# Kernel optimization log

Hardware: AMD Instinct MI355X
Metric: run time of the kernel (lower is better)

Reference implementation:

```python
import jax, jax.numpy as jnp
import numpy as np

N_NODES = 100000
N_EDGES = 1600000
HIDDEN = 128


def setup_inputs() -> dict:
    key = jax.random.key(0)
    k1, k2, k3, k4 = jax.random.split(key, 4)
    x = jax.random.normal(k1, (N_NODES, HIDDEN), dtype=jnp.float32)
    edge_index = jax.random.randint(k2, (2, N_EDGES), 0, N_NODES, dtype=jnp.int64)
    edge_weight = jax.random.uniform(k3, (N_EDGES,), dtype=jnp.float32)
    W_att = jax.random.normal(k4, (1, HIDDEN), dtype=jnp.float32) * (1.0 / np.sqrt(HIDDEN))
    b_att = jnp.zeros((1,), dtype=jnp.float32)
    return {"x": x, "edge_index": edge_index, "edge_weight": edge_weight,
            "W_att": W_att, "b_att": b_att}


def reference(x, edge_index, edge_weight, W_att, b_att):
    row, col = edge_index[0], edge_index[1]
    # per-node attention score in (0,1): sigmoid(Linear(x))  -> [N]
    scores = jax.nn.sigmoid(x @ W_att.T + b_att)[:, 0]
    # per-edge energy: gather endpoints, multiply by edge weight  -> [E]
    energy = scores[row] * scores[col] * edge_weight
    # GLOBAL softmax over all edges (dim=0 in torch)  -> [E]
    attn = jax.nn.softmax(energy)
    # scatter-add weighted source features into row nodes  -> [N, H]
    out = jax.ops.segment_sum(x[col] * attn[:, None], row, num_segments=x.shape[0])
    return out
```

## Files before the change

### kernel.cpp

```cpp
#include <hip/hip_runtime.h>
#include <math.h>

#define N_NODES  100000
#define N_EDGES  1600000
#define HIDDEN   128
#define CAP      32
#define OVF_CAP  8192

__global__ void scores_kernel(const float* __restrict__ x,
                              const float* __restrict__ W,
                              const float* __restrict__ b,
                              float* __restrict__ scores) {
    int gwave = (blockIdx.x * blockDim.x + threadIdx.x) >> 6;
    int lane  = threadIdx.x & 63;
    if (gwave >= N_NODES) return;
    const float2 xv = *reinterpret_cast<const float2*>(x + (size_t)gwave * HIDDEN + lane * 2);
    const float2 wv = *reinterpret_cast<const float2*>(W + lane * 2);
    float d = xv.x * wv.x + xv.y * wv.y;
#pragma unroll
    for (int off = 32; off > 0; off >>= 1)
        d += __shfl_xor(d, off, 64);
    if (lane == 0) {
        float z = d + b[0];
        scores[gwave] = 1.0f / (1.0f + expf(-z));
    }
}

__global__ void energy_bucket_kernel(const int* __restrict__ ei,
                                     const float* __restrict__ ew,
                                     const float* __restrict__ scores,
                                     double* __restrict__ sum,
                                     int* __restrict__ cnt,
                                     float2* __restrict__ ebuf,
                                     int* __restrict__ ovf_cnt,
                                     float4* __restrict__ ovf) {
    int e4 = blockIdx.x * blockDim.x + threadIdx.x;
    double local = 0.0;
    if (e4 < N_EDGES / 4) {
        int4   r4 = reinterpret_cast<const int4*>(ei)[e4];
        int4   c4 = reinterpret_cast<const int4*>(ei + N_EDGES)[e4];
        float4 w4 = reinterpret_cast<const float4*>(ew)[e4];
        int   rs[4] = {r4.x, r4.y, r4.z, r4.w};
        int   cs[4] = {c4.x, c4.y, c4.z, c4.w};
        float wsv[4] = {w4.x, w4.y, w4.z, w4.w};
#pragma unroll
        for (int k = 0; k < 4; ++k) {
            int r = rs[k], c = cs[k];
            float pe = expf(scores[r] * scores[c] * wsv[k]);
            local += (double)pe;
            int pos = atomicAdd(&cnt[r], 1);
            if (pos < CAP) {
                ebuf[(size_t)r * CAP + pos] = make_float2(__int_as_float(c), pe);
            } else {
                int oi = atomicAdd(ovf_cnt, 1);
                if (oi < OVF_CAP)
                    ovf[oi] = make_float4(__int_as_float(r), __int_as_float(c), pe, 0.f);
            }
        }
    }
#pragma unroll
    for (int off = 32; off > 0; off >>= 1)
        local += __shfl_xor(local, off, 64);
    __shared__ double part[4];
    int lane = threadIdx.x & 63, w = threadIdx.x >> 6;
    if (lane == 0) part[w] = local;
    __syncthreads();
    if (threadIdx.x == 0)
        atomicAdd(sum, part[0] + part[1] + part[2] + part[3]);
}

__global__ void accumulate_kernel(const float* __restrict__ x,
                                  const int* __restrict__ cnt,
                                  const float2* __restrict__ ebuf,
                                  const double* __restrict__ sum,
                                  float* __restrict__ out) {
    int n    = (blockIdx.x * blockDim.x + threadIdx.x) >> 6;
    int lane = threadIdx.x & 63;
    if (n >= N_NODES) return;
    int deg = cnt[n];
    if (deg > CAP) deg = CAP;
    const float4* rec4 = reinterpret_cast<const float4*>(ebuf + (size_t)n * CAP);
    float a0 = 0.f, a1 = 0.f;
    int j = 0;
    for (; j + 4 <= deg; j += 4) {
        float4 q0 = rec4[(j >> 1)];
        float4 q1 = rec4[(j >> 1) + 1];
        const float2 x0 = *reinterpret_cast<const float2*>(x + (size_t)__float_as_int(q0.x) * HIDDEN + lane * 2);
        const float2 x1 = *reinterpret_cast<const float2*>(x + (size_t)__float_as_int(q0.z) * HIDDEN + lane * 2);
        const float2 x2 = *reinterpret_cast<const float2*>(x + (size_t)__float_as_int(q1.x) * HIDDEN + lane * 2);
        const float2 x3 = *reinterpret_cast<const float2*>(x + (size_t)__float_as_int(q1.z) * HIDDEN + lane * 2);
        a0 += x0.x * q0.y; a1 += x0.y * q0.y;
        a0 += x1.x * q0.w; a1 += x1.y * q0.w;
        a0 += x2.x * q1.y; a1 += x2.y * q1.y;
        a0 += x3.x * q1.w; a1 += x3.y * q1.w;
    }
    const float2* rec = ebuf + (size_t)n * CAP;
    for (; j < deg; ++j) {
        float2 r = rec[j];
        const float2 xv = *reinterpret_cast<const float2*>(x + (size_t)__float_as_int(r.x) * HIDDEN + lane * 2);
        a0 += xv.x * r.y; a1 += xv.y * r.y;
    }
    float inv = (float)(1.0 / sum[0]);
    *reinterpret_cast<float2*>(out + (size_t)n * HIDDEN + lane * 2) =
        make_float2(a0 * inv, a1 * inv);
}

__global__ void overflow_kernel(const float* __restrict__ x,
                                const float4* __restrict__ ovf,
                                const int* __restrict__ ovf_cnt,
                                const double* __restrict__ sum,
                                float* __restrict__ out) {
    int cnt = *ovf_cnt;
    if (cnt > OVF_CAP) cnt = OVF_CAP;
    float inv = (float)(1.0 / sum[0]);
    int wid  = (blockIdx.x * blockDim.x + threadIdx.x) >> 6;
    int lane = threadIdx.x & 63;
    int nw   = (gridDim.x * blockDim.x) >> 6;
    for (int i = wid; i < cnt; i += nw) {
        float4 rc = ovf[i];
        int r = __float_as_int(rc.x);
        int c = __float_as_int(rc.y);
        float a = rc.z * inv;
        const float2 xv = *reinterpret_cast<const float2*>(x + (size_t)c * HIDDEN + lane * 2);
        float* o = out + (size_t)r * HIDDEN + lane * 2;
        atomicAdd(o,     xv.x * a);
        atomicAdd(o + 1, xv.y * a);
    }
}

extern "C" void kernel_launch(void* const* d_in, const int* in_sizes, int n_in,
                              void* d_out, int out_size, void* d_ws, size_t ws_size,
                              hipStream_t stream) {
    const float* x   = (const float*)d_in[0];
    const int*   ei  = (const int*)d_in[1];
    const float* ew  = (const float*)d_in[2];
    const float* W   = (const float*)d_in[3];
    const float* b   = (const float*)d_in[4];
    float*       out = (float*)d_out;

    char* ws = (char*)d_ws;
    double* sum     = (double*)ws;
    int*    ovf_cnt = (int*)(ws + 8);
    int*    cnt     = (int*)(ws + 16);
    float*  scores  = (float*)(ws + 400016);
    float4* ovf     = (float4*)(ws + 800016);
    float2* ebuf    = (float2*)(ws + 931088);

    hipMemsetAsync(ws, 0, 16 + N_NODES * sizeof(int), stream);

    scores_kernel<<<(N_NODES + 3) / 4, 256, 0, stream>>>(x, W, b, scores);
    energy_bucket_kernel<<<(N_EDGES / 4 + 255) / 256, 256, 0, stream>>>(
        ei, ew, scores, sum, cnt, ebuf, ovf_cnt, ovf);
    accumulate_kernel<<<(N_NODES + 3) / 4, 256, 0, stream>>>(x, cnt, ebuf, sum, out);
    overflow_kernel<<<16, 256, 0, stream>>>(x, ovf, ovf_cnt, sum, out);
}
```

Baseline: 321.2 us.

## Fuse count reset into scores, widen edge loads, half-wave float4 gather accumulate

```diff
diff --git a/kernel.cpp b/kernel.cpp
--- a/kernel.cpp
+++ b/kernel.cpp
@@ -7,22 +7,29 @@
 #define CAP      32
 #define OVF_CAP  8192
 
+typedef int   vi4 __attribute__((ext_vector_type(4)));
+typedef float vf4 __attribute__((ext_vector_type(4)));
+typedef float vf2 __attribute__((ext_vector_type(2)));
+
 __global__ void scores_kernel(const float* __restrict__ x,
                               const float* __restrict__ W,
                               const float* __restrict__ b,
-                              float* __restrict__ scores) {
-    int gwave = (blockIdx.x * blockDim.x + threadIdx.x) >> 6;
-    int lane  = threadIdx.x & 63;
-    if (gwave >= N_NODES) return;
-    const float2 xv = *reinterpret_cast<const float2*>(x + (size_t)gwave * HIDDEN + lane * 2);
-    const float2 wv = *reinterpret_cast<const float2*>(W + lane * 2);
-    float d = xv.x * wv.x + xv.y * wv.y;
+                              float* __restrict__ scores,
+                              int* __restrict__ cnt) {
+    int wave = (blockIdx.x * blockDim.x + threadIdx.x) >> 6;
+    int lane = threadIdx.x & 63;
+    int h = lane >> 5, l32 = lane & 31;
+    int n = wave * 2 + h;
+    if (n >= N_NODES) return;
+    float4 xv = *reinterpret_cast<const float4*>(x + (size_t)n * HIDDEN + l32 * 4);
+    float4 wv = *reinterpret_cast<const float4*>(W + l32 * 4);
+    float d = xv.x * wv.x + xv.y * wv.y + xv.z * wv.z + xv.w * wv.w;
 #pragma unroll
-    for (int off = 32; off > 0; off >>= 1)
+    for (int off = 16; off > 0; off >>= 1)
         d += __shfl_xor(d, off, 64);
-    if (lane == 0) {
-        float z = d + b[0];
-        scores[gwave] = 1.0f / (1.0f + expf(-z));
+    if (l32 == 0) {
+        scores[n] = 1.0f / (1.0f + expf(-(d + b[0])));
+        cnt[n] = 0;
     }
 }
 
@@ -31,26 +38,34 @@
                                      const float* __restrict__ scores,
                                      double* __restrict__ sum,
                                      int* __restrict__ cnt,
-                                     float2* __restrict__ ebuf,
+                                     float* __restrict__ ebuf,
                                      int* __restrict__ ovf_cnt,
                                      float4* __restrict__ ovf) {
-    int e4 = blockIdx.x * blockDim.x + threadIdx.x;
+    int t = blockIdx.x * blockDim.x + threadIdx.x;
     double local = 0.0;
-    if (e4 < N_EDGES / 4) {
-        int4   r4 = reinterpret_cast<const int4*>(ei)[e4];
-        int4   c4 = reinterpret_cast<const int4*>(ei + N_EDGES)[e4];
-        float4 w4 = reinterpret_cast<const float4*>(ew)[e4];
-        int   rs[4] = {r4.x, r4.y, r4.z, r4.w};
-        int   cs[4] = {c4.x, c4.y, c4.z, c4.w};
-        float wsv[4] = {w4.x, w4.y, w4.z, w4.w};
+    if (t < N_EDGES / 8) {
+        const vi4* ri = reinterpret_cast<const vi4*>(ei);
+        const vi4* ci = reinterpret_cast<const vi4*>(ei + N_EDGES);
+        const vf4* wi = reinterpret_cast<const vf4*>(ew);
+        vi4 ra = __builtin_nontemporal_load(ri + 2 * t);
+        vi4 rb = __builtin_nontemporal_load(ri + 2 * t + 1);
+        vi4 ca = __builtin_nontemporal_load(ci + 2 * t);
+        vi4 cb = __builtin_nontemporal_load(ci + 2 * t + 1);
+        vf4 wa = __builtin_nontemporal_load(wi + 2 * t);
+        vf4 wb = __builtin_nontemporal_load(wi + 2 * t + 1);
+        int   rs[8] = {ra.x, ra.y, ra.z, ra.w, rb.x, rb.y, rb.z, rb.w};
+        int   cs[8] = {ca.x, ca.y, ca.z, ca.w, cb.x, cb.y, cb.z, cb.w};
+        float wsv[8] = {wa.x, wa.y, wa.z, wa.w, wb.x, wb.y, wb.z, wb.w};
 #pragma unroll
-        for (int k = 0; k < 4; ++k) {
+        for (int k = 0; k < 8; ++k) {
             int r = rs[k], c = cs[k];
             float pe = expf(scores[r] * scores[c] * wsv[k]);
             local += (double)pe;
             int pos = atomicAdd(&cnt[r], 1);
             if (pos < CAP) {
-                ebuf[(size_t)r * CAP + pos] = make_float2(__int_as_float(c), pe);
+                vf2 recv; recv.x = __int_as_float(c); recv.y = pe;
+                __builtin_nontemporal_store(recv,
+                    reinterpret_cast<vf2*>(ebuf + ((size_t)r * CAP + pos) * 2));
             } else {
                 int oi = atomicAdd(ovf_cnt, 1);
                 if (oi < OVF_CAP)
@@ -79,30 +94,40 @@
     if (n >= N_NODES) return;
     int deg = cnt[n];
     if (deg > CAP) deg = CAP;
-    const float4* rec4 = reinterpret_cast<const float4*>(ebuf + (size_t)n * CAP);
-    float a0 = 0.f, a1 = 0.f;
+    int h = lane >> 5, l32 = lane & 31;
+    const float2* rec = ebuf + (size_t)n * CAP;
+    float4 acc = make_float4(0.f, 0.f, 0.f, 0.f);
     int j = 0;
-    for (; j + 4 <= deg; j += 4) {
-        float4 q0 = rec4[(j >> 1)];
-        float4 q1 = rec4[(j >> 1) + 1];
-        const float2 x0 = *reinterpret_cast<const float2*>(x + (size_t)__float_as_int(q0.x) * HIDDEN + lane * 2);
-        const float2 x1 = *reinterpret_cast<const float2*>(x + (size_t)__float_as_int(q0.z) * HIDDEN + lane * 2);
-        const float2 x2 = *reinterpret_cast<const float2*>(x + (size_t)__float_as_int(q1.x) * HIDDEN + lane * 2);
-        const float2 x3 = *reinterpret_cast<const float2*>(x + (size_t)__float_as_int(q1.z) * HIDDEN + lane * 2);
-        a0 += x0.x * q0.y; a1 += x0.y * q0.y;
-        a0 += x1.x * q0.w; a1 += x1.y * q0.w;
-        a0 += x2.x * q1.y; a1 += x2.y * q1.y;
-        a0 += x3.x * q1.w; a1 += x3.y * q1.w;
+    for (; j + 8 <= deg; j += 8) {
+        float2 r0 = rec[j + h];
+        float2 r1 = rec[j + 2 + h];
+        float2 r2 = rec[j + 4 + h];
+        float2 r3 = rec[j + 6 + h];
+        const float4 x0 = *reinterpret_cast<const float4*>(x + (size_t)__float_as_int(r0.x) * HIDDEN + l32 * 4);
+        const float4 x1 = *reinterpret_cast<const float4*>(x + (size_t)__float_as_int(r1.x) * HIDDEN + l32 * 4);
+        const float4 x2 = *reinterpret_cast<const float4*>(x + (size_t)__float_as_int(r2.x) * HIDDEN + l32 * 4);
+        const float4 x3 = *reinterpret_cast<const float4*>(x + (size_t)__float_as_int(r3.x) * HIDDEN + l32 * 4);
+        acc.x += x0.x * r0.y; acc.y += x0.y * r0.y; acc.z += x0.z * r0.y; acc.w += x0.w * r0.y;
+        acc.x += x1.x * r1.y; acc.y += x1.y * r1.y; acc.z += x1.z * r1.y; acc.w += x1.w * r1.y;
+        acc.x += x2.x * r2.y; acc.y += x2.y * r2.y; acc.z += x2.z * r2.y; acc.w += x2.w * r2.y;
+        acc.x += x3.x * r3.y; acc.y += x3.y * r3.y; acc.z += x3.z * r3.y; acc.w += x3.w * r3.y;
     }
-    const float2* rec = ebuf + (size_t)n * CAP;
-    for (; j < deg; ++j) {
-        float2 r = rec[j];
-        const float2 xv = *reinterpret_cast<const float2*>(x + (size_t)__float_as_int(r.x) * HIDDEN + lane * 2);
-        a0 += xv.x * r.y; a1 += xv.y * r.y;
+    for (; j < deg; j += 2) {
+        if (j + h < deg) {
+            float2 r0 = rec[j + h];
+            const float4 x0 = *reinterpret_cast<const float4*>(x + (size_t)__float_as_int(r0.x) * HIDDEN + l32 * 4);
+            acc.x += x0.x * r0.y; acc.y += x0.y * r0.y; acc.z += x0.z * r0.y; acc.w += x0.w * r0.y;
+        }
     }
-    float inv = (float)(1.0 / sum[0]);
-    *reinterpret_cast<float2*>(out + (size_t)n * HIDDEN + lane * 2) =
-        make_float2(a0 * inv, a1 * inv);
+    acc.x += __shfl_xor(acc.x, 32, 64);
+    acc.y += __shfl_xor(acc.y, 32, 64);
+    acc.z += __shfl_xor(acc.z, 32, 64);
+    acc.w += __shfl_xor(acc.w, 32, 64);
+    if (h == 0) {
+        float inv = (float)(1.0 / sum[0]);
+        acc.x *= inv; acc.y *= inv; acc.z *= inv; acc.w *= inv;
+        *reinterpret_cast<float4*>(out + (size_t)n * HIDDEN + l32 * 4) = acc;
+    }
 }
 
 __global__ void overflow_kernel(const float* __restrict__ x,
@@ -144,13 +169,14 @@
     int*    cnt     = (int*)(ws + 16);
     float*  scores  = (float*)(ws + 400016);
     float4* ovf     = (float4*)(ws + 800016);
-    float2* ebuf    = (float2*)(ws + 931088);
+    float*  ebuf    = (float*)(ws + 931088);
 
-    hipMemsetAsync(ws, 0, 16 + N_NODES * sizeof(int), stream);
+    (void)hipMemsetAsync(ws, 0, 16, stream);
 
-    scores_kernel<<<(N_NODES + 3) / 4, 256, 0, stream>>>(x, W, b, scores);
-    energy_bucket_kernel<<<(N_EDGES / 4 + 255) / 256, 256, 0, stream>>>(
+    scores_kernel<<<(N_NODES + 7) / 8, 256, 0, stream>>>(x, W, b, scores, cnt);
+    energy_bucket_kernel<<<(N_EDGES / 8 + 255) / 256, 256, 0, stream>>>(
         ei, ew, scores, sum, cnt, ebuf, ovf_cnt, ovf);
-    accumulate_kernel<<<(N_NODES + 3) / 4, 256, 0, stream>>>(x, cnt, ebuf, sum, out);
+    accumulate_kernel<<<(N_NODES + 3) / 4, 256, 0, stream>>>(
+        x, cnt, reinterpret_cast<const float2*>(ebuf), sum, out);
     overflow_kernel<<<16, 256, 0, stream>>>(x, ovf, ovf_cnt, sum, out);
 }
```

New measurement: 316.3 us. About the same (-1.5%).
